# Optimization experiments

Measured on AMD Instinct MI355X. Metric: run time of the kernel, lower is better.

The kernel has to match this reference:

```python
import jax, jax.numpy as jnp
import numpy as np
from functools import partial

SEQ, BATCH, IN, HID = 512, 128, 256, 1024


def setup_inputs() -> dict:
    key = jax.random.key(0)
    ks = jax.random.split(key, 8)
    std = 1.0 / np.sqrt(HID)
    u = lambda k, shape: jax.random.uniform(k, shape, jnp.float32, -std, std)
    return {
        "inp": jax.random.normal(ks[0], (SEQ, BATCH, IN), jnp.float32),
        "Wxh": u(ks[1], (4 * HID, IN)),
        "bxh": u(ks[2], (4 * HID,)),
        "Whh": u(ks[3], (4 * HID, HID)),
        "bhh": u(ks[4], (4 * HID,)),
        "Wout": u(ks[5], (IN, HID)),
        "bout": u(ks[6], (IN,)),
    }


def lstm_forward(inp, Wxh, bxh, Whh, bhh, Wout, bout):
    seq, batch, _ = inp.shape
    hid = Whh.shape[1]
    # Precompute input projection for all timesteps: [T, B, 4H]
    x_proj = jnp.einsum("tbi,gi->tbg", inp, Wxh) + bxh

    def step(carry, xp_t):
        h, c = carry
        gates = xp_t + h @ Whh.T + bhh            # [B, 4H]
        i, f, g, o = jnp.split(gates, 4, axis=-1)  # torch chunk order: i,f,g,o
        c = jax.nn.sigmoid(f) * c + jax.nn.sigmoid(i) * jnp.tanh(g)
        h = jax.nn.sigmoid(o) * jnp.tanh(c)
        return (h, c), h

    h0 = jnp.zeros((batch, hid), inp.dtype)
    c0 = jnp.zeros((batch, hid), inp.dtype)
    _, hs = jax.lax.scan(step, (h0, c0), x_proj)   # hs: [T, B, H]
    out = jnp.einsum("tbh,ih->tbi", hs, Wout) + bout
    return jax.nn.log_softmax(out, axis=-1)


def reference(inp, Wxh, bxh, Whh, bhh, Wout, bout):
    return lstm_forward(inp, Wxh, bxh, Whh, bhh, Wout, bout)
```

## Files before the change

### kernel.cpp

```cpp
#include <hip/hip_runtime.h>
#include <math.h>


#define TT  512
#define BB  128
#define NIN 256
#define NH  1024
#define G4  4096
#define KK  1280

typedef __bf16 bf16_t;
typedef bf16_t bf16x8 __attribute__((ext_vector_type(8)));
typedef float  f32x4  __attribute__((ext_vector_type(4)));

#define MFMA(a, b, c) __builtin_amdgcn_mfma_f32_16x16x32_bf16((a), (b), (c), 0, 0, 0)


__global__ void conv_w_kernel(const float* __restrict__ Wxh,
                              const float* __restrict__ Whh,
                              bf16_t* __restrict__ Wc) {
  const int n = blockIdx.y;
  const int k = blockIdx.x * 256 + threadIdx.x;
  const int g = n & 3, j = n >> 2;
  float v = (k < NIN) ? Wxh[(size_t)(g * NH + j) * NIN + k]
                      : Whh[(size_t)(g * NH + j) * NH + (k - NIN)];
  Wc[(size_t)n * KK + k] = (bf16_t)v;
}

__global__ void conv_f2b_kernel(const float* __restrict__ src,
                                bf16_t* __restrict__ dst, int n4) {
  int i = blockIdx.x * 256 + threadIdx.x;
  if (i < n4) {
    float4 v = ((const float4*)src)[i];
    dst[i * 4 + 0] = (bf16_t)v.x;
    dst[i * 4 + 1] = (bf16_t)v.y;
    dst[i * 4 + 2] = (bf16_t)v.z;
    dst[i * 4 + 3] = (bf16_t)v.w;
  }
}

__global__ void prep_bias_kernel(const float* __restrict__ bxh,
                                 const float* __restrict__ bhh,
                                 float* __restrict__ bsum4) {
  int n = blockIdx.x * 256 + threadIdx.x;
  int g = n & 3, j = n >> 2;
  bsum4[n] = bxh[g * NH + j] + bhh[g * NH + j];
}


__global__ __launch_bounds__(512) void fused_step(
    int t,
    const bf16_t* __restrict__ x_bf,
    const bf16_t* __restrict__ Wc,
    const float*  __restrict__ bsum4,
    const bf16_t* __restrict__ h_cur,
    bf16_t*       __restrict__ h_next,
    float*        __restrict__ c,
    const bf16_t* __restrict__ WoutB,
    const float*  __restrict__ bout,
    float*        __restrict__ logits_w,
    const float*  __restrict__ logits_r,
    float*        __restrict__ out)
{
  const int blk  = blockIdx.x;
  const int tid  = threadIdx.x;
  const int lane = tid & 63;
  const int wv   = tid >> 6;
  const int l16  = lane & 15;
  const int lq   = lane >> 4;

  if (blk < 128) {
    if (t >= TT) return;
    __shared__ float gs[2][64 * 68];

    const int mb    = (blk & 1) * 64;
    const int ns    = blk >> 1;
    const int nbase = ns * 64;
    const int wm = wv & 1, wn = (wv >> 1) & 1, kh = wv >> 2;
    const int m0 = mb + wm * 32;
    const int n0 = nbase + wn * 32;

    const bf16_t* ax  = x_bf + (size_t)t * BB * NIN + (size_t)(m0 + l16) * NIN + lq * 8;
    const bf16_t* ah  = h_cur + (size_t)(m0 + l16) * NH + lq * 8;
    const bf16_t* b0p = Wc + (size_t)(n0 + l16) * KK + lq * 8;
    const bf16_t* b1p = Wc + (size_t)(n0 + 16 + l16) * KK + lq * 8;

    f32x4 a00 = {0,0,0,0}, a01 = {0,0,0,0}, a10 = {0,0,0,0}, a11 = {0,0,0,0};

    if (kh == 0) {
#pragma unroll
      for (int kk = 0; kk < 8; ++kk) {
        bf16x8 r0 = *(const bf16x8*)(ax + kk * 32);
        bf16x8 r1 = *(const bf16x8*)(ax + 16 * NIN + kk * 32);
        bf16x8 b0 = *(const bf16x8*)(b0p + kk * 32);
        bf16x8 b1 = *(const bf16x8*)(b1p + kk * 32);
        a00 = MFMA(r0, b0, a00); a01 = MFMA(r0, b1, a01);
        a10 = MFMA(r1, b0, a10); a11 = MFMA(r1, b1, a11);
      }
#pragma unroll 6
      for (int kk = 0; kk < 12; ++kk) {
        bf16x8 r0 = *(const bf16x8*)(ah + kk * 32);
        bf16x8 r1 = *(const bf16x8*)(ah + 16 * NH + kk * 32);
        bf16x8 b0 = *(const bf16x8*)(b0p + NIN + kk * 32);
        bf16x8 b1 = *(const bf16x8*)(b1p + NIN + kk * 32);
        a00 = MFMA(r0, b0, a00); a01 = MFMA(r0, b1, a01);
        a10 = MFMA(r1, b0, a10); a11 = MFMA(r1, b1, a11);
      }
    } else {
#pragma unroll 5
      for (int kk = 12; kk < 32; ++kk) {
        bf16x8 r0 = *(const bf16x8*)(ah + kk * 32);
        bf16x8 r1 = *(const bf16x8*)(ah + 16 * NH + kk * 32);
        bf16x8 b0 = *(const bf16x8*)(b0p + NIN + kk * 32);
        bf16x8 b1 = *(const bf16x8*)(b1p + NIN + kk * 32);
        a00 = MFMA(r0, b0, a00); a01 = MFMA(r0, b1, a01);
        a10 = MFMA(r1, b0, a10); a11 = MFMA(r1, b1, a11);
      }
    }

    float* g = gs[kh];
#pragma unroll
    for (int r = 0; r < 4; ++r) {
      const int rr0 = wm * 32 + lq * 4 + r;
      g[rr0 * 68 + wn * 32 + l16]             = a00[r];
      g[rr0 * 68 + wn * 32 + 16 + l16]        = a01[r];
      g[(rr0 + 16) * 68 + wn * 32 + l16]      = a10[r];
      g[(rr0 + 16) * 68 + wn * 32 + 16 + l16] = a11[r];
    }
    __syncthreads();

    const int b_l = tid >> 3;
#pragma unroll
    for (int p = 0; p < 2; ++p) {
      const int jl = (tid & 7) + p * 8;
      const int j  = ns * 16 + jl;
      float4 g0 = *(const float4*)&gs[0][b_l * 68 + jl * 4];
      float4 g1 = *(const float4*)&gs[1][b_l * 68 + jl * 4];
      float4 bs = ((const float4*)bsum4)[j];
      const float gi = g0.x + g1.x + bs.x;
      const float gf = g0.y + g1.y + bs.y;
      const float gg = g0.z + g1.z + bs.z;
      const float go = g0.w + g1.w + bs.w;
      const float si = 1.f / (1.f + __expf(-gi));
      const float sf = 1.f / (1.f + __expf(-gf));
      const float so = 1.f / (1.f + __expf(-go));
      const size_t idx = (size_t)(mb + b_l) * NH + j;
      const float cn = sf * c[idx] + si * tanhf(gg);
      c[idx] = cn;
      h_next[idx] = (bf16_t)(so * tanhf(cn));
    }
  } else if (blk < 144) {
    if (t < 1 || t > TT) return;
    const int gw  = (blk - 128) * 8 + wv;
    const int bm0 = (gw >> 4) * 16;
    const int bn0 = (gw & 15) * 16;

    const bf16_t* ap = h_cur + (size_t)(bm0 + l16) * NH + lq * 8;
    const bf16_t* bp = WoutB + (size_t)(bn0 + l16) * NH + lq * 8;
    f32x4 acc = {0,0,0,0};
#pragma unroll 8
    for (int kk = 0; kk < 32; ++kk) {
      bf16x8 a = *(const bf16x8*)(ap + kk * 32);
      bf16x8 b = *(const bf16x8*)(bp + kk * 32);
      acc = MFMA(a, b, acc);
    }
    const float bo = bout[bn0 + l16];
#pragma unroll
    for (int r = 0; r < 4; ++r)
      logits_w[(size_t)(bm0 + lq * 4 + r) * NIN + bn0 + l16] = acc[r] + bo;
  } else {
    if (t < 2) return;
    __shared__ float red[2][2][4][4];
    const int sub  = tid >> 8;
    const int stid = tid & 255;
    const int swv  = (tid >> 6) & 3;
    const int b0 = (blk - 144) * 8 + sub * 4;
    float v[4], mx[4], sm[4];
#pragma unroll
    for (int r = 0; r < 4; ++r) v[r] = logits_r[(size_t)(b0 + r) * NIN + stid];
#pragma unroll
    for (int r = 0; r < 4; ++r) mx[r] = v[r];
#pragma unroll
    for (int off = 32; off > 0; off >>= 1)
#pragma unroll
      for (int r = 0; r < 4; ++r) mx[r] = fmaxf(mx[r], __shfl_xor(mx[r], off));
    if (lane == 0)
#pragma unroll
      for (int r = 0; r < 4; ++r) red[0][sub][swv][r] = mx[r];
    __syncthreads();
#pragma unroll
    for (int r = 0; r < 4; ++r)
      mx[r] = fmaxf(fmaxf(red[0][sub][0][r], red[0][sub][1][r]),
                    fmaxf(red[0][sub][2][r], red[0][sub][3][r]));
#pragma unroll
    for (int r = 0; r < 4; ++r) sm[r] = __expf(v[r] - mx[r]);
#pragma unroll
    for (int off = 32; off > 0; off >>= 1)
#pragma unroll
      for (int r = 0; r < 4; ++r) sm[r] += __shfl_xor(sm[r], off);
    if (lane == 0)
#pragma unroll
      for (int r = 0; r < 4; ++r) red[1][sub][swv][r] = sm[r];
    __syncthreads();
    float* ot = out + (size_t)(t - 2) * BB * NIN + (size_t)b0 * NIN;
#pragma unroll
    for (int r = 0; r < 4; ++r) {
      float S = red[1][sub][0][r] + red[1][sub][1][r] +
                red[1][sub][2][r] + red[1][sub][3][r];
      ot[(size_t)r * NIN + stid] = v[r] - mx[r] - logf(S);
    }
  }
}


extern "C" void kernel_launch(void* const* d_in, const int* in_sizes, int n_in,
                              void* d_out, int out_size, void* d_ws, size_t ws_size,
                              hipStream_t stream) {
  const float* inp  = (const float*)d_in[0];
  const float* Wxh  = (const float*)d_in[1];
  const float* bxh  = (const float*)d_in[2];
  const float* Whh  = (const float*)d_in[3];
  const float* bhh  = (const float*)d_in[4];
  const float* Wout = (const float*)d_in[5];
  const float* bout = (const float*)d_in[6];
  float* out = (float*)d_out;

  char* p = (char*)d_ws;
  bf16_t* Wc    = (bf16_t*)p; p += (size_t)G4 * KK * 2;
  bf16_t* x_bf  = (bf16_t*)p; p += (size_t)TT * BB * NIN * 2;
  bf16_t* WoutB = (bf16_t*)p; p += (size_t)NIN * NH * 2;
  bf16_t* h0    = (bf16_t*)p; p += (size_t)BB * NH * 2;
  bf16_t* h1    = (bf16_t*)p; p += (size_t)BB * NH * 2;
  float*  cbuf  = (float*)p;  p += (size_t)BB * NH * 4;
  float*  bsum4 = (float*)p;  p += (size_t)G4 * 4;
  float*  lg0   = (float*)p;  p += (size_t)BB * NIN * 4;
  float*  lg1   = (float*)p;  p += (size_t)BB * NIN * 4;

  conv_w_kernel<<<dim3(KK / 256, G4), 256, 0, stream>>>(Wxh, Whh, Wc);
  conv_f2b_kernel<<<(TT * BB * NIN / 4 + 255) / 256, 256, 0, stream>>>(
      inp, x_bf, TT * BB * NIN / 4);
  conv_f2b_kernel<<<(NIN * NH / 4 + 255) / 256, 256, 0, stream>>>(
      Wout, WoutB, NIN * NH / 4);
  prep_bias_kernel<<<G4 / 256, 256, 0, stream>>>(bxh, bhh, bsum4);
  hipMemsetAsync(h0, 0, (size_t)BB * NH * 2, stream);
  hipMemsetAsync(cbuf, 0, (size_t)BB * NH * 4, stream);

  bf16_t* hb[2] = {h0, h1};
  float*  lg[2] = {lg0, lg1};
  for (int t = 0; t < TT + 2; ++t) {
    fused_step<<<160, 512, 0, stream>>>(
        t, x_bf, Wc, bsum4,
        hb[t & 1], hb[(t + 1) & 1], cbuf,
        WoutB, bout,
        lg[t & 1],
        lg[(t + 1) & 1],
        out);
  }
}
```

Baseline: 10.82 ms.

## Replace per-timestep kernel launches with persistent kernel and grid barrier

The 514 per-timestep launches are folded into one persistent kernel of 160 blocks that loops over time. Blocks synchronize through a hand-written grid barrier built from atomics: counters are spread over 8 padded slots, and block 0 gathers them and publishes an epoch. This removes launch overhead and the inter-kernel gaps on the serial recurrence. The cost is that every block must be co-resident, and a spin-wait bailout bounded by an iteration count could silently break ordering if a wait times out.

```diff
diff --git a/kernel.cpp b/kernel.cpp
--- a/kernel.cpp
+++ b/kernel.cpp
@@ -8,6 +8,7 @@
 #define NH  1024
 #define G4  4096
 #define KK  1280
+#define NBLK 160
 
 typedef __bf16 bf16_t;
 typedef bf16_t bf16x8 __attribute__((ext_vector_type(8)));
@@ -48,19 +49,20 @@
 }
 
 
-__global__ __launch_bounds__(512) void fused_step(
-    int t,
+__global__ __launch_bounds__(512) void lstm_persist(
     const bf16_t* __restrict__ x_bf,
     const bf16_t* __restrict__ Wc,
     const float*  __restrict__ bsum4,
-    const bf16_t* __restrict__ h_cur,
-    bf16_t*       __restrict__ h_next,
-    float*        __restrict__ c,
+    bf16_t*       __restrict__ hb0,
+    bf16_t*       __restrict__ hb1,
+    float*        __restrict__ cbuf,
     const bf16_t* __restrict__ WoutB,
     const float*  __restrict__ bout,
-    float*        __restrict__ logits_w,
-    const float*  __restrict__ logits_r,
-    float*        __restrict__ out)
+    float*        __restrict__ lgb0,
+    float*        __restrict__ lgb1,
+    float*        __restrict__ out,
+    int* barcnt,
+    int* barep)
 {
   const int blk  = blockIdx.x;
   const int tid  = threadIdx.x;
@@ -69,145 +71,186 @@
   const int l16  = lane & 15;
   const int lq   = lane >> 4;
 
-  if (blk < 128) {
-    if (t >= TT) return;
-    __shared__ float gs[2][64 * 68];
-
-    const int mb    = (blk & 1) * 64;
-    const int ns    = blk >> 1;
-    const int nbase = ns * 64;
-    const int wm = wv & 1, wn = (wv >> 1) & 1, kh = wv >> 2;
-    const int m0 = mb + wm * 32;
-    const int n0 = nbase + wn * 32;
-
-    const bf16_t* ax  = x_bf + (size_t)t * BB * NIN + (size_t)(m0 + l16) * NIN + lq * 8;
-    const bf16_t* ah  = h_cur + (size_t)(m0 + l16) * NH + lq * 8;
-    const bf16_t* b0p = Wc + (size_t)(n0 + l16) * KK + lq * 8;
-    const bf16_t* b1p = Wc + (size_t)(n0 + 16 + l16) * KK + lq * 8;
-
-    f32x4 a00 = {0,0,0,0}, a01 = {0,0,0,0}, a10 = {0,0,0,0}, a11 = {0,0,0,0};
-
-    if (kh == 0) {
-#pragma unroll
-      for (int kk = 0; kk < 8; ++kk) {
-        bf16x8 r0 = *(const bf16x8*)(ax + kk * 32);
-        bf16x8 r1 = *(const bf16x8*)(ax + 16 * NIN + kk * 32);
-        bf16x8 b0 = *(const bf16x8*)(b0p + kk * 32);
-        bf16x8 b1 = *(const bf16x8*)(b1p + kk * 32);
-        a00 = MFMA(r0, b0, a00); a01 = MFMA(r0, b1, a01);
-        a10 = MFMA(r1, b0, a10); a11 = MFMA(r1, b1, a11);
-      }
+  __shared__ float gs[2][64 * 68];
+  __shared__ float red[2][2][4][4];
+
+  const int mb    = (blk & 1) * 64;
+  const int ns    = blk >> 1;
+  const int nbase = ns * 64;
+  const int wm = wv & 1, wn = (wv >> 1) & 1, kh = wv >> 2;
+  const int m0 = mb + wm * 32;
+  const int n0 = nbase + wn * 32;
+
+  for (int t = 0; t <= TT + 1; ++t) {
+    const bf16_t* h_cur  = (t & 1) ? hb1 : hb0;
+    bf16_t*       h_next = (t & 1) ? hb0 : hb1;
+    float*        lgw    = (t & 1) ? lgb1 : lgb0;
+    const float*  lgr    = (t & 1) ? lgb0 : lgb1;
+
+    if (blk < 128 && t < TT) {
+      const bf16_t* ax  = x_bf + (size_t)t * BB * NIN + (size_t)(m0 + l16) * NIN + lq * 8;
+      const bf16_t* ah  = h_cur + (size_t)(m0 + l16) * NH + lq * 8;
+      const bf16_t* b0p = Wc + (size_t)(n0 + l16) * KK + lq * 8;
+      const bf16_t* b1p = Wc + (size_t)(n0 + 16 + l16) * KK + lq * 8;
+
+      f32x4 a00 = {0,0,0,0}, a01 = {0,0,0,0}, a10 = {0,0,0,0}, a11 = {0,0,0,0};
+
+      if (kh == 0) {
+#pragma unroll
+        for (int kk = 0; kk < 8; ++kk) {
+          bf16x8 r0 = *(const bf16x8*)(ax + kk * 32);
+          bf16x8 r1 = *(const bf16x8*)(ax + 16 * NIN + kk * 32);
+          bf16x8 b0 = *(const bf16x8*)(b0p + kk * 32);
+          bf16x8 b1 = *(const bf16x8*)(b1p + kk * 32);
+          a00 = MFMA(r0, b0, a00); a01 = MFMA(r0, b1, a01);
+          a10 = MFMA(r1, b0, a10); a11 = MFMA(r1, b1, a11);
+        }
 #pragma unroll 6
-      for (int kk = 0; kk < 12; ++kk) {
-        bf16x8 r0 = *(const bf16x8*)(ah + kk * 32);
-        bf16x8 r1 = *(const bf16x8*)(ah + 16 * NH + kk * 32);
-        bf16x8 b0 = *(const bf16x8*)(b0p + NIN + kk * 32);
-        bf16x8 b1 = *(const bf16x8*)(b1p + NIN + kk * 32);
-        a00 = MFMA(r0, b0, a00); a01 = MFMA(r0, b1, a01);
-        a10 = MFMA(r1, b0, a10); a11 = MFMA(r1, b1, a11);
-      }
-    } else {
+        for (int kk = 0; kk < 12; ++kk) {
+          bf16x8 r0 = *(const bf16x8*)(ah + kk * 32);
+          bf16x8 r1 = *(const bf16x8*)(ah + 16 * NH + kk * 32);
+          bf16x8 b0 = *(const bf16x8*)(b0p + NIN + kk * 32);
+          bf16x8 b1 = *(const bf16x8*)(b1p + NIN + kk * 32);
+          a00 = MFMA(r0, b0, a00); a01 = MFMA(r0, b1, a01);
+          a10 = MFMA(r1, b0, a10); a11 = MFMA(r1, b1, a11);
+        }
+      } else {
 #pragma unroll 5
-      for (int kk = 12; kk < 32; ++kk) {
-        bf16x8 r0 = *(const bf16x8*)(ah + kk * 32);
-        bf16x8 r1 = *(const bf16x8*)(ah + 16 * NH + kk * 32);
-        bf16x8 b0 = *(const bf16x8*)(b0p + NIN + kk * 32);
-        bf16x8 b1 = *(const bf16x8*)(b1p + NIN + kk * 32);
-        a00 = MFMA(r0, b0, a00); a01 = MFMA(r0, b1, a01);
-        a10 = MFMA(r1, b0, a10); a11 = MFMA(r1, b1, a11);
+        for (int kk = 12; kk < 32; ++kk) {
+          bf16x8 r0 = *(const bf16x8*)(ah + kk * 32);
+          bf16x8 r1 = *(const bf16x8*)(ah + 16 * NH + kk * 32);
+          bf16x8 b0 = *(const bf16x8*)(b0p + NIN + kk * 32);
+          bf16x8 b1 = *(const bf16x8*)(b1p + NIN + kk * 32);
+          a00 = MFMA(r0, b0, a00); a01 = MFMA(r0, b1, a01);
+          a10 = MFMA(r1, b0, a10); a11 = MFMA(r1, b1, a11);
+        }
+      }
+
+      float* g = gs[kh];
+#pragma unroll
+      for (int r = 0; r < 4; ++r) {
+        const int rr0 = wm * 32 + lq * 4 + r;
+        g[rr0 * 68 + wn * 32 + l16]             = a00[r];
+        g[rr0 * 68 + wn * 32 + 16 + l16]        = a01[r];
+        g[(rr0 + 16) * 68 + wn * 32 + l16]      = a10[r];
+        g[(rr0 + 16) * 68 + wn * 32 + 16 + l16] = a11[r];
+      }
+      __syncthreads();
+
+      const int b_l = tid >> 3;
+#pragma unroll
+      for (int p = 0; p < 2; ++p) {
+        const int jl = (tid & 7) + p * 8;
+        const int j  = ns * 16 + jl;
+        float4 g0 = *(const float4*)&gs[0][b_l * 68 + jl * 4];
+        float4 g1 = *(const float4*)&gs[1][b_l * 68 + jl * 4];
+        float4 bs = ((const float4*)bsum4)[j];
+        const float gi = g0.x + g1.x + bs.x;
+        const float gf = g0.y + g1.y + bs.y;
+        const float gg = g0.z + g1.z + bs.z;
+        const float go = g0.w + g1.w + bs.w;
+        const float si = 1.f / (1.f + __expf(-gi));
+        const float sf = 1.f / (1.f + __expf(-gf));
+        const float so = 1.f / (1.f + __expf(-go));
+        const size_t idx = (size_t)(mb + b_l) * NH + j;
+        const float cn = sf * cbuf[idx] + si * tanhf(gg);
+        cbuf[idx] = cn;
+        h_next[idx] = (bf16_t)(so * tanhf(cn));
+      }
+    } else if (blk >= 128 && blk < 144 && t >= 1 && t <= TT) {
+      const int gw  = (blk - 128) * 8 + wv;
+      const int bm0 = (gw >> 4) * 16;
+      const int bn0 = (gw & 15) * 16;
+
+      const bf16_t* ap = h_cur + (size_t)(bm0 + l16) * NH + lq * 8;
+      const bf16_t* bp = WoutB + (size_t)(bn0 + l16) * NH + lq * 8;
+      f32x4 acc = {0,0,0,0};
+#pragma unroll 8
+      for (int kk = 0; kk < 32; ++kk) {
+        bf16x8 a = *(const bf16x8*)(ap + kk * 32);
+        bf16x8 b = *(const bf16x8*)(bp + kk * 32);
+        acc = MFMA(a, b, acc);
+      }
+      const float bo = bout[bn0 + l16];
+#pragma unroll
+      for (int r = 0; r < 4; ++r)
+        lgw[(size_t)(bm0 + lq * 4 + r) * NIN + bn0 + l16] = acc[r] + bo;
+    } else if (blk >= 144 && t >= 2) {
+      const int sub  = tid >> 8;
+      const int stid = tid & 255;
+      const int swv  = (tid >> 6) & 3;
+      const int b0 = (blk - 144) * 8 + sub * 4;
+      float v[4], mx[4], sm[4];
+#pragma unroll
+      for (int r = 0; r < 4; ++r) v[r] = lgr[(size_t)(b0 + r) * NIN + stid];
+#pragma unroll
+      for (int r = 0; r < 4; ++r) mx[r] = v[r];
+#pragma unroll
+      for (int off = 32; off > 0; off >>= 1)
+#pragma unroll
+        for (int r = 0; r < 4; ++r) mx[r] = fmaxf(mx[r], __shfl_xor(mx[r], off));
+      if (lane == 0)
+#pragma unroll
+        for (int r = 0; r < 4; ++r) red[0][sub][swv][r] = mx[r];
+      __syncthreads();
+#pragma unroll
+      for (int r = 0; r < 4; ++r)
+        mx[r] = fmaxf(fmaxf(red[0][sub][0][r], red[0][sub][1][r]),
+                      fmaxf(red[0][sub][2][r], red[0][sub][3][r]));
+#pragma unroll
+      for (int r = 0; r < 4; ++r) sm[r] = __expf(v[r] - mx[r]);
+#pragma unroll
+      for (int off = 32; off > 0; off >>= 1)
+#pragma unroll
+        for (int r = 0; r < 4; ++r) sm[r] += __shfl_xor(sm[r], off);
+      if (lane == 0)
+#pragma unroll
+        for (int r = 0; r < 4; ++r) red[1][sub][swv][r] = sm[r];
+      __syncthreads();
+      float* ot = out + (size_t)(t - 2) * BB * NIN + (size_t)b0 * NIN;
+#pragma unroll
+      for (int r = 0; r < 4; ++r) {
+        float S = red[1][sub][0][r] + red[1][sub][1][r] +
+                  red[1][sub][2][r] + red[1][sub][3][r];
+        ot[(size_t)r * NIN + stid] = v[r] - mx[r] - logf(S);
       }
     }
 
-    float* g = gs[kh];
-#pragma unroll
-    for (int r = 0; r < 4; ++r) {
-      const int rr0 = wm * 32 + lq * 4 + r;
-      g[rr0 * 68 + wn * 32 + l16]             = a00[r];
-      g[rr0 * 68 + wn * 32 + 16 + l16]        = a01[r];
-      g[(rr0 + 16) * 68 + wn * 32 + l16]      = a10[r];
-      g[(rr0 + 16) * 68 + wn * 32 + 16 + l16] = a11[r];
-    }
-    __syncthreads();
-
-    const int b_l = tid >> 3;
-#pragma unroll
-    for (int p = 0; p < 2; ++p) {
-      const int jl = (tid & 7) + p * 8;
-      const int j  = ns * 16 + jl;
-      float4 g0 = *(const float4*)&gs[0][b_l * 68 + jl * 4];
-      float4 g1 = *(const float4*)&gs[1][b_l * 68 + jl * 4];
-      float4 bs = ((const float4*)bsum4)[j];
-      const float gi = g0.x + g1.x + bs.x;
-      const float gf = g0.y + g1.y + bs.y;
-      const float gg = g0.z + g1.z + bs.z;
-      const float go = g0.w + g1.w + bs.w;
-      const float si = 1.f / (1.f + __expf(-gi));
-      const float sf = 1.f / (1.f + __expf(-gf));
-      const float so = 1.f / (1.f + __expf(-go));
-      const size_t idx = (size_t)(mb + b_l) * NH + j;
-      const float cn = sf * c[idx] + si * tanhf(gg);
-      c[idx] = cn;
-      h_next[idx] = (bf16_t)(so * tanhf(cn));
-    }
-  } else if (blk < 144) {
-    if (t < 1 || t > TT) return;
-    const int gw  = (blk - 128) * 8 + wv;
-    const int bm0 = (gw >> 4) * 16;
-    const int bn0 = (gw & 15) * 16;
-
-    const bf16_t* ap = h_cur + (size_t)(bm0 + l16) * NH + lq * 8;
-    const bf16_t* bp = WoutB + (size_t)(bn0 + l16) * NH + lq * 8;
-    f32x4 acc = {0,0,0,0};
-#pragma unroll 8
-    for (int kk = 0; kk < 32; ++kk) {
-      bf16x8 a = *(const bf16x8*)(ap + kk * 32);
-      bf16x8 b = *(const bf16x8*)(bp + kk * 32);
-      acc = MFMA(a, b, acc);
-    }
-    const float bo = bout[bn0 + l16];
-#pragma unroll
-    for (int r = 0; r < 4; ++r)
-      logits_w[(size_t)(bm0 + lq * 4 + r) * NIN + bn0 + l16] = acc[r] + bo;
-  } else {
-    if (t < 2) return;
-    __shared__ float red[2][2][4][4];
-    const int sub  = tid >> 8;
-    const int stid = tid & 255;
-    const int swv  = (tid >> 6) & 3;
-    const int b0 = (blk - 144) * 8 + sub * 4;
-    float v[4], mx[4], sm[4];
-#pragma unroll
-    for (int r = 0; r < 4; ++r) v[r] = logits_r[(size_t)(b0 + r) * NIN + stid];
-#pragma unroll
-    for (int r = 0; r < 4; ++r) mx[r] = v[r];
-#pragma unroll
-    for (int off = 32; off > 0; off >>= 1)
-#pragma unroll
-      for (int r = 0; r < 4; ++r) mx[r] = fmaxf(mx[r], __shfl_xor(mx[r], off));
-    if (lane == 0)
-#pragma unroll
-      for (int r = 0; r < 4; ++r) red[0][sub][swv][r] = mx[r];
-    __syncthreads();
-#pragma unroll
-    for (int r = 0; r < 4; ++r)
-      mx[r] = fmaxf(fmaxf(red[0][sub][0][r], red[0][sub][1][r]),
-                    fmaxf(red[0][sub][2][r], red[0][sub][3][r]));
-#pragma unroll
-    for (int r = 0; r < 4; ++r) sm[r] = __expf(v[r] - mx[r]);
-#pragma unroll
-    for (int off = 32; off > 0; off >>= 1)
-#pragma unroll
-      for (int r = 0; r < 4; ++r) sm[r] += __shfl_xor(sm[r], off);
-    if (lane == 0)
-#pragma unroll
-      for (int r = 0; r < 4; ++r) red[1][sub][swv][r] = sm[r];
-    __syncthreads();
-    float* ot = out + (size_t)(t - 2) * BB * NIN + (size_t)b0 * NIN;
-#pragma unroll
-    for (int r = 0; r < 4; ++r) {
-      float S = red[1][sub][0][r] + red[1][sub][1][r] +
-                red[1][sub][2][r] + red[1][sub][3][r];
-      ot[(size_t)r * NIN + stid] = v[r] - mx[r] - logf(S);
+    if (t <= TT) {
+      const int ep = t + 1;
+      __syncthreads();
+      if (blk == 0) {
+        if (tid < 8) {
+          if (tid == 0) __threadfence();
+          const int tgt = ((tid == 0) ? 19 : 20) * ep;
+          int gcnt = 0;
+          while (__hip_atomic_load(&barcnt[tid << 5], __ATOMIC_RELAXED,
+                                   __HIP_MEMORY_SCOPE_AGENT) < tgt) {
+            __builtin_amdgcn_s_sleep(1);
+            if (++gcnt > (1 << 22)) break;
+          }
+        }
+        __syncthreads();
+        if (tid == 0) {
+          __builtin_amdgcn_fence(__ATOMIC_ACQUIRE, "agent");
+          __hip_atomic_store(barep, ep, __ATOMIC_RELEASE, __HIP_MEMORY_SCOPE_AGENT);
+        }
+        __syncthreads();
+      } else {
+        if (tid == 0) {
+          __threadfence();
+          __hip_atomic_fetch_add(&barcnt[(blk & 7) << 5], 1, __ATOMIC_RELAXED,
+                                 __HIP_MEMORY_SCOPE_AGENT);
+          int gcnt = 0;
+          while (__hip_atomic_load(barep, __ATOMIC_RELAXED,
+                                   __HIP_MEMORY_SCOPE_AGENT) < ep) {
+            __builtin_amdgcn_s_sleep(1);
+            if (++gcnt > (1 << 22)) break;
+          }
+          __builtin_amdgcn_fence(__ATOMIC_ACQUIRE, "agent");
+        }
+        __syncthreads();
+      }
     }
   }
 }
@@ -222,7 +265,7 @@
   const float* Whh  = (const float*)d_in[3];
   const float* bhh  = (const float*)d_in[4];
   const float* Wout = (const float*)d_in[5];
-  const float* bout = (const float*)d_in[6];
+  const float* boutp= (const float*)d_in[6];
   float* out = (float*)d_out;
 
   char* p = (char*)d_ws;
@@ -235,6 +278,8 @@
   float*  bsum4 = (float*)p;  p += (size_t)G4 * 4;
   float*  lg0   = (float*)p;  p += (size_t)BB * NIN * 4;
   float*  lg1   = (float*)p;  p += (size_t)BB * NIN * 4;
+  int*    barcnt= (int*)p;    p += 8 * 32 * 4;
+  int*    barep = (int*)p;    p += 32 * 4;
 
   conv_w_kernel<<<dim3(KK / 256, G4), 256, 0, stream>>>(Wxh, Whh, Wc);
   conv_f2b_kernel<<<(TT * BB * NIN / 4 + 255) / 256, 256, 0, stream>>>(
@@ -244,16 +289,9 @@
   prep_bias_kernel<<<G4 / 256, 256, 0, stream>>>(bxh, bhh, bsum4);
   hipMemsetAsync(h0, 0, (size_t)BB * NH * 2, stream);
   hipMemsetAsync(cbuf, 0, (size_t)BB * NH * 4, stream);
-
-  bf16_t* hb[2] = {h0, h1};
-  float*  lg[2] = {lg0, lg1};
-  for (int t = 0; t < TT + 2; ++t) {
-    fused_step<<<160, 512, 0, stream>>>(
-        t, x_bf, Wc, bsum4,
-        hb[t & 1], hb[(t + 1) & 1], cbuf,
-        WoutB, bout,
-        lg[t & 1],
-        lg[(t + 1) & 1],
-        out);
-  }
-}
+  hipMemsetAsync(barcnt, 0, (8 * 32 + 32) * 4, stream);
+
+  lstm_persist<<<NBLK, 512, 0, stream>>>(
+      x_bf, Wc, bsum4, h0, h1, cbuf, WoutB, boutp, lg0, lg1, out,
+      barcnt, barep);
+}
```

Result: slower. 12.83 ms (+18.5%).
